# Kernel tuning notes

Measured on AMD Instinct MI355X. Metric: run time of the kernel, lower is better.

Reference implementation:

```python
import jax, jax.numpy as jnp
import numpy as np

MODEL_DIM = 256
NUM_HEAD = 8
HEAD_DIM = MODEL_DIM // NUM_HEAD  # 32
ROT_DIM_AXIS = int(0.5 * HEAD_DIM)  # 16 per axis, 32 total rotated channels
LN_EPS = 1e-5
MASK_BIAS = -1e9  # fp32 precision
SCALE = HEAD_DIM ** -0.5
INIT_RANGE = 0.02
N_LAYERS = 6


def _rotate_half(x):
    # interleaved pairs: (d r) with r=2 -> (-x2, x1) re-interleaved
    x = x.reshape(*x.shape[:-1], -1, 2)
    x1, x2 = x[..., 0], x[..., 1]
    return jnp.stack([-x2, x1], axis=-1).reshape(*x.shape[:-2], -1)


def _axial_freqs(seqlen):
    # RotaryEmbedding('lang' freqs) over t = linspace(-1, 1, seqlen)
    inv_freq = 1.0 / (10000.0 ** (jnp.arange(0, ROT_DIM_AXIS, 2, dtype=jnp.float32) / ROT_DIM_AXIS))
    t = jnp.linspace(-1.0, 1.0, seqlen, dtype=jnp.float32)
    f = jnp.repeat(t[:, None] * inv_freq[None, :], 2, axis=-1)  # (s, ROT_DIM_AXIS)
    fh = jnp.broadcast_to(f[:, None, :], (seqlen, seqlen, ROT_DIM_AXIS))
    fw = jnp.broadcast_to(f[None, :, :], (seqlen, seqlen, ROT_DIM_AXIS))
    return jnp.concatenate([fh, fw], axis=-1)  # (s, s, 2*ROT_DIM_AXIS)


def _apply_rotary(freqs, t):
    rot_dim = freqs.shape[-1]
    t_rot, t_pass = t[..., :rot_dim], t[..., rot_dim:]
    t_rot = t_rot * jnp.cos(freqs) + _rotate_half(t_rot) * jnp.sin(freqs)
    return jnp.concatenate([t_rot, t_pass], axis=-1)


def setup_inputs() -> dict:
    key = jax.random.key(0)
    k1, k2, k3, k4 = jax.random.split(key, 4)
    b, s = 2, 128
    pair_act = jax.random.normal(k1, (b, s, s, MODEL_DIM), dtype=jnp.float32)
    pair_mask = jax.random.randint(k2, (b, s, s), 0, 2).astype(bool)  # True = masked
    Wqkv = jax.random.normal(k3, (3 * MODEL_DIM, MODEL_DIM), dtype=jnp.float32) * INIT_RANGE
    Wout = jax.random.normal(k4, (MODEL_DIM, MODEL_DIM), dtype=jnp.float32) * (INIT_RANGE / np.sqrt(2 * N_LAYERS))
    ln_gamma = jnp.ones((MODEL_DIM,), dtype=jnp.float32)
    ln_beta = jnp.zeros((MODEL_DIM,), dtype=jnp.float32)
    return {"pair_act": pair_act, "pair_mask": pair_mask, "ln_gamma": ln_gamma,
            "ln_beta": ln_beta, "Wqkv": Wqkv, "Wout": Wout}


def reference(pair_act, pair_mask, ln_gamma, ln_beta, Wqkv, Wout):
    # orientation == 'per_row': no axis swap
    b, s = pair_act.shape[0], pair_act.shape[1]
    # LayerNorm over model_dim
    mu = jnp.mean(pair_act, axis=-1, keepdims=True)
    var = jnp.var(pair_act, axis=-1, keepdims=True)
    x = (pair_act - mu) * jax.lax.rsqrt(var + LN_EPS) * ln_gamma + ln_beta
    # QKV projection (no bias)
    qkv = jnp.einsum('bxyd,ed->bxye', x, Wqkv)  # (b, s, s, 3*MODEL_DIM)
    q, k, v = jnp.split(qkv, 3, axis=-1)
    # 2D axial rotary on first 2*ROT_DIM_AXIS channels of the feature dim
    freqs = _axial_freqs(s)  # (s, s, 32)
    q = _apply_rotary(freqs, q)
    k = _apply_rotary(freqs, k)
    # multihead attention per row (axis s1 independent)
    q = q.reshape(b, s, s, NUM_HEAD, HEAD_DIM)
    k = k.reshape(b, s, s, NUM_HEAD, HEAD_DIM)
    v = v.reshape(b, s, s, NUM_HEAD, HEAD_DIM)
    scores = jnp.einsum('bxqhd,bxkhd->bxhqk', q, k) * SCALE  # (b, s1, h, s2, s2)
    mask = pair_mask[:, :, None, None, :]  # (b, s1, 1, 1, s2)
    scores = jnp.where(mask, MASK_BIAS, scores)
    attn = jax.nn.softmax(scores, axis=-1)
    out = jnp.einsum('bxhqk,bxkhd->bxqhd', attn, v).reshape(b, s, s, MODEL_DIM)
    return jnp.einsum('bxyd,ed->bxye', out, Wout)
```

## Files before the change

kernel.cpp:

```cpp
#include <hip/hip_runtime.h>
#include <math.h>
#include <stdint.h>

typedef __attribute__((ext_vector_type(8))) short short8;
typedef __attribute__((ext_vector_type(4))) short short4v;
typedef __attribute__((ext_vector_type(4))) float floatx4;

#define SEQ 128
#define DM 256
#define NQKV 768
#define LN_EPS 1e-5f
#define ATT_SCALE 0.17677669529663687f

__device__ __constant__ float INVF[8] = {
    1.0f, 0.31622776601683794f, 0.1f, 0.031622776601683794f,
    0.01f, 0.0031622776601683794f, 0.001f, 0.00031622776601683794f};

__device__ inline unsigned short f2bf(float f) {
    unsigned u = __float_as_uint(f);
    u += 0x7fffu + ((u >> 16) & 1u);
    return (unsigned short)(u >> 16);
}

__device__ inline void gl_lds16(const unsigned short* g, unsigned short* l) {
    __builtin_amdgcn_global_load_lds(
        (const __attribute__((address_space(1))) void*)(uintptr_t)g,
        (__attribute__((address_space(3))) void*)(uintptr_t)l, 16, 0, 0);
}

__global__ __launch_bounds__(256)
void prep_kernel(const float* __restrict__ pa, const float* __restrict__ gamma,
                 const float* __restrict__ beta, unsigned short* __restrict__ xln,
                 const float* __restrict__ wq, const float* __restrict__ wo,
                 unsigned short* __restrict__ bq, unsigned short* __restrict__ bo) {
    int bid = blockIdx.x;
    int tid = threadIdx.x;
    if (bid < 8192) {
        int lane = tid & 63, wid = tid >> 6;
        int row = bid * 4 + wid;
        float4 v = *(const float4*)(pa + (size_t)row * DM + lane * 4);
        float s = v.x + v.y + v.z + v.w;
        #pragma unroll
        for (int o = 32; o > 0; o >>= 1) s += __shfl_xor(s, o);
        float mean = s * (1.0f / DM);
        float d0 = v.x - mean, d1 = v.y - mean, d2 = v.z - mean, d3 = v.w - mean;
        float sq = d0 * d0 + d1 * d1 + d2 * d2 + d3 * d3;
        #pragma unroll
        for (int o = 32; o > 0; o >>= 1) sq += __shfl_xor(sq, o);
        float r = rsqrtf(sq * (1.0f / DM) + LN_EPS);
        float4 g = *(const float4*)(gamma + lane * 4);
        float4 b = *(const float4*)(beta + lane * 4);
        short4v o4;
        o4[0] = (short)f2bf(d0 * r * g.x + b.x);
        o4[1] = (short)f2bf(d1 * r * g.y + b.y);
        o4[2] = (short)f2bf(d2 * r * g.z + b.z);
        o4[3] = (short)f2bf(d3 * r * g.w + b.w);
        *(short4v*)(xln + (size_t)row * DM + lane * 4) = o4;
    } else {
        int e = bid - 8192;
        bq[e * DM + tid] = f2bf(wq[e * DM + tid]);
        if (e < DM) bo[e * DM + tid] = f2bf(wo[e * DM + tid]);
    }
}

template <bool OUTBF16, bool ROT>
__global__ __launch_bounds__(256)
void gemm_mfma(const unsigned short* __restrict__ A,
               const unsigned short* __restrict__ B,
               void* __restrict__ Cout, int N) {
    __shared__ __align__(16) unsigned short As[128 * 64];
    __shared__ __align__(16) unsigned short Bs[128 * 64];
    int m0 = blockIdx.x * 128, n0 = blockIdx.y * 128;
    int tid = threadIdx.x;
    int wave = tid >> 6, lane = tid & 63, qd = lane >> 4, lo = lane & 15;
    int wm = (wave & 1) * 64, wn = (wave >> 1) * 64;

    floatx4 acc[4][4];
    #pragma unroll
    for (int i = 0; i < 4; ++i)
        #pragma unroll
        for (int j = 0; j < 4; ++j) acc[i][j] = (floatx4){0.f, 0.f, 0.f, 0.f};

    int rsub = lane >> 3;
    int csub = (lane & 7) ^ rsub;

    for (int k0 = 0; k0 < 256; k0 += 64) {
        #pragma unroll
        for (int t = 0; t < 4; ++t) {
            int rbase = (wave * 4 + t) * 8;
            int row = rbase + rsub;
            gl_lds16(A + (size_t)(m0 + row) * 256 + k0 + csub * 8, &As[rbase * 64]);
            gl_lds16(B + (size_t)(n0 + row) * 256 + k0 + csub * 8, &Bs[rbase * 64]);
        }
        __syncthreads();
        #pragma unroll
        for (int kk = 0; kk < 64; kk += 32) {
            int kkc = kk >> 3;
            short8 af[4], bf[4];
            #pragma unroll
            for (int t = 0; t < 4; ++t) {
                int row = wm + t * 16 + lo;
                int sc = (kkc + qd) ^ (row & 7);
                af[t] = *(const short8*)&As[row * 64 + sc * 8];
            }
            #pragma unroll
            for (int t = 0; t < 4; ++t) {
                int row = wn + t * 16 + lo;
                int sc = (kkc + qd) ^ (row & 7);
                bf[t] = *(const short8*)&Bs[row * 64 + sc * 8];
            }
            #pragma unroll
            for (int i = 0; i < 4; ++i)
                #pragma unroll
                for (int j = 0; j < 4; ++j)
                    acc[i][j] = __builtin_amdgcn_mfma_f32_16x16x32_bf16(
                        af[i], bf[j], acc[i][j], 0, 0, 0);
        }
        __syncthreads();
    }

    if (ROT) {
        #pragma unroll
        for (int j = 0; j < 4; ++j) {
            int gcb = n0 + wn + j * 16;
            int sect = gcb >> 5;
            if (sect == 0 || sect == 8) {
                int p = (((j & 1) * 16) + lo) >> 1;
                float invf = INVF[p & 7];
                float sgn = (lo & 1) ? 1.0f : -1.0f;
                #pragma unroll
                for (int i = 0; i < 4; ++i) {
                    #pragma unroll
                    for (int r = 0; r < 4; ++r) {
                        int grow = m0 + wm + i * 16 + qd * 4 + r;
                        int yy = grow & 127, xx = (grow >> 7) & 127;
                        float tpos = (p < 8) ? (-1.0f + (2.0f / 127.0f) * (float)xx)
                                             : (-1.0f + (2.0f / 127.0f) * (float)yy);
                        float th = tpos * invf;
                        float sn, cs;
                        __sincosf(th, &sn, &cs);
                        float v = acc[i][j][r];
                        float pv = __shfl_xor(v, 1);
                        acc[i][j][r] = v * cs + sgn * pv * sn;
                    }
                }
            }
        }
    }

    #pragma unroll
    for (int i = 0; i < 4; ++i) {
        int growb = m0 + wm + i * 16 + qd * 4;
        #pragma unroll
        for (int j = 0; j < 4; ++j) {
            int gc = n0 + wn + j * 16 + lo;
            #pragma unroll
            for (int r = 0; r < 4; ++r) {
                float v = acc[i][j][r];
                int grow = growb + r;
                if (OUTBF16) {
                    unsigned b = f2bf(v);
                    unsigned other = (unsigned)__shfl_xor((int)b, 1) & 0xffffu;
                    if ((lo & 1) == 0) {
                        unsigned pk = b | (other << 16);
                        *(unsigned*)((unsigned short*)Cout + (size_t)grow * N + gc) = pk;
                    }
                } else {
                    ((float*)Cout)[(size_t)grow * N + gc] = v;
                }
            }
        }
    }
}

__global__ __launch_bounds__(256)
void attn_mfma(const unsigned short* __restrict__ qkv, const int* __restrict__ mask,
               unsigned short* __restrict__ attn_out) {
    __shared__ __align__(16) unsigned short Vt[32 * 136];
    __shared__ __align__(16) unsigned short Ps[128 * 136];

    int blk = blockIdx.x;
    int h = blk & 7, bx = blk >> 3;
    int tid = threadIdx.x;
    int wave = tid >> 6, lane = tid & 63, qd = lane >> 4, lo = lane & 15;
    const unsigned short* base = qkv + (size_t)bx * SEQ * NQKV;

    {
        int row = tid >> 1, half = tid & 1;
        const unsigned short* vp = base + row * NQKV + 512 + h * 32 + half * 16;
        short8 v0 = *(const short8*)vp;
        short8 v1 = *(const short8*)(vp + 8);
        #pragma unroll
        for (int j = 0; j < 8; ++j) {
            Vt[(half * 16 + j) * 136 + row] = (unsigned short)v0[j];
            Vt[(half * 16 + 8 + j) * 136 + row] = (unsigned short)v1[j];
        }
    }
    __syncthreads();

    int m0 = wave * 32;

    short8 aq[2];
    #pragma unroll
    for (int t = 0; t < 2; ++t)
        aq[t] = *(const short8*)(base + (m0 + t * 16 + lo) * NQKV + h * 32 + qd * 8);

    float msel[8];
    #pragma unroll
    for (int nt = 0; nt < 8; ++nt)
        msel[nt] = mask[bx * SEQ + nt * 16 + lo] ? 0.0f : 1.0f;

    float s[2][4] = {};
    #pragma unroll
    for (int nt = 0; nt < 8; ++nt) {
        short8 bk = *(const short8*)(base + (nt * 16 + lo) * NQKV + 256 + h * 32 + qd * 8);
        #pragma unroll
        for (int t = 0; t < 2; ++t) {
            floatx4 c = (floatx4){0.f, 0.f, 0.f, 0.f};
            c = __builtin_amdgcn_mfma_f32_16x16x32_bf16(aq[t], bk, c, 0, 0, 0);
            #pragma unroll
            for (int r = 0; r < 4; ++r) {
                float e = __expf(c[r] * ATT_SCALE) * msel[nt];
                s[t][r] += e;
                Ps[(m0 + t * 16 + qd * 4 + r) * 136 + nt * 16 + lo] = f2bf(e);
            }
        }
    }

    float inv[2][4];
    #pragma unroll
    for (int t = 0; t < 2; ++t)
        #pragma unroll
        for (int r = 0; r < 4; ++r) {
            float v = s[t][r];
            v += __shfl_xor(v, 1);
            v += __shfl_xor(v, 2);
            v += __shfl_xor(v, 4);
            v += __shfl_xor(v, 8);
            inv[t][r] = 1.0f / v;
        }

    floatx4 o[2][2];
    #pragma unroll
    for (int t = 0; t < 2; ++t)
        #pragma unroll
        for (int n = 0; n < 2; ++n) o[t][n] = (floatx4){0.f, 0.f, 0.f, 0.f};
    #pragma unroll
    for (int k0 = 0; k0 < 4; ++k0) {
        short8 pa[2], vb[2];
        #pragma unroll
        for (int t = 0; t < 2; ++t)
            pa[t] = *(const short8*)&Ps[(m0 + t * 16 + lo) * 136 + k0 * 32 + qd * 8];
        #pragma unroll
        for (int n = 0; n < 2; ++n)
            vb[n] = *(const short8*)&Vt[(n * 16 + lo) * 136 + k0 * 32 + qd * 8];
        #pragma unroll
        for (int t = 0; t < 2; ++t)
            #pragma unroll
            for (int n = 0; n < 2; ++n)
                o[t][n] = __builtin_amdgcn_mfma_f32_16x16x32_bf16(
                    pa[t], vb[n], o[t][n], 0, 0, 0);
    }

    #pragma unroll
    for (int t = 0; t < 2; ++t)
        #pragma unroll
        for (int r = 0; r < 4; ++r) {
            int qrow = m0 + t * 16 + qd * 4 + r;
            float iv = inv[t][r];
            #pragma unroll
            for (int n = 0; n < 2; ++n) {
                float v = o[t][n][r] * iv;
                unsigned b = f2bf(v);
                unsigned other = (unsigned)__shfl_xor((int)b, 1) & 0xffffu;
                if ((lo & 1) == 0) {
                    unsigned pk = b | (other << 16);
                    *(unsigned*)&attn_out[((size_t)bx * SEQ + qrow) * DM +
                                          h * 32 + n * 16 + lo] = pk;
                }
            }
        }
}

extern "C" void kernel_launch(void* const* d_in, const int* in_sizes, int n_in,
                              void* d_out, int out_size, void* d_ws, size_t ws_size,
                              hipStream_t stream) {
    const float* pair_act = (const float*)d_in[0];
    const int* pair_mask = (const int*)d_in[1];
    const float* ln_gamma = (const float*)d_in[2];
    const float* ln_beta = (const float*)d_in[3];
    const float* Wqkv = (const float*)d_in[4];
    const float* Wout = (const float*)d_in[5];
    float* out = (float*)d_out;

    char* ws = (char*)d_ws;
    unsigned short* qkv_bf = (unsigned short*)ws;
    unsigned short* xln_bf = (unsigned short*)(ws + 50331648);
    unsigned short* attn_bf = (unsigned short*)(ws + 67108864);
    unsigned short* wqkv_bf = (unsigned short*)(ws + 83886080);
    unsigned short* wout_bf = (unsigned short*)(ws + 84279296);

    const int R = 2 * SEQ * SEQ;

    prep_kernel<<<8960, 256, 0, stream>>>(pair_act, ln_gamma, ln_beta, xln_bf,
                                          Wqkv, Wout, wqkv_bf, wout_bf);
    gemm_mfma<true, true><<<dim3(R / 128, NQKV / 128), 256, 0, stream>>>(
        xln_bf, wqkv_bf, qkv_bf, NQKV);
    attn_mfma<<<2 * SEQ * 8, 256, 0, stream>>>(qkv_bf, pair_mask, attn_bf);
    gemm_mfma<false, false><<<dim3(R / 128, DM / 128), 256, 0, stream>>>(
        attn_bf, wout_bf, out, DM);
}
```

Before: 151.0 us.

## Fuse LayerNorm, QKV projection, attention and output projection into one per-row kernel

Replaces the four-kernel pipeline with a small weight-conversion kernel and a single fused kernel. Each block of 512 threads handles one attention row of 128 tokens and keeps LayerNorm output, Q/K/V, attention output and the output projection in registers and LDS. This removes the global round-trips for the bf16 LN activations, the QKV tensor and the attention output. In exchange, only 256 blocks are launched, register pressure is high, and the weight tiles are reloaded into LDS by every block with many barriers per block.

Result: slower. 156.9 us (+3.9%).

```diff
diff --git a/kernel.cpp b/kernel.cpp
--- a/kernel.cpp
+++ b/kernel.cpp
@@ -3,12 +3,8 @@
 #include <stdint.h>
 
 typedef __attribute__((ext_vector_type(8))) short short8;
-typedef __attribute__((ext_vector_type(4))) short short4v;
 typedef __attribute__((ext_vector_type(4))) float floatx4;
 
-#define SEQ 128
-#define DM 256
-#define NQKV 768
 #define LN_EPS 1e-5f
 #define ATT_SCALE 0.17677669529663687f
 
@@ -29,257 +25,280 @@
 }
 
 __global__ __launch_bounds__(256)
-void prep_kernel(const float* __restrict__ pa, const float* __restrict__ gamma,
-                 const float* __restrict__ beta, unsigned short* __restrict__ xln,
-                 const float* __restrict__ wq, const float* __restrict__ wo,
-                 unsigned short* __restrict__ bq, unsigned short* __restrict__ bo) {
-    int bid = blockIdx.x;
+void prep_w(const float* __restrict__ wq, const float* __restrict__ wo,
+            unsigned short* __restrict__ bq, unsigned short* __restrict__ bo) {
+    int g = blockIdx.x * 256 + threadIdx.x;
+    const float* src;
+    unsigned short* dst;
+    if (g < 49152) { src = wq + (size_t)g * 4; dst = bq + (size_t)g * 4; }
+    else { int h = g - 49152; src = wo + (size_t)h * 4; dst = bo + (size_t)h * 4; }
+    float4 v = *(const float4*)src;
+    uint2 o;
+    o.x = (unsigned)f2bf(v.x) | ((unsigned)f2bf(v.y) << 16);
+    o.y = (unsigned)f2bf(v.z) | ((unsigned)f2bf(v.w) << 16);
+    *(uint2*)dst = o;
+}
+
+__global__ __launch_bounds__(512, 2)
+void fused_kernel(const float* __restrict__ pair_act, const int* __restrict__ mask,
+                  const float* __restrict__ gamma, const float* __restrict__ beta,
+                  const unsigned short* __restrict__ Wqkv,
+                  const unsigned short* __restrict__ Wout,
+                  float* __restrict__ out) {
+    __shared__ __align__(16) unsigned char smem[61952];
+    unsigned short* S16 = (unsigned short*)smem;
+    unsigned short* Ks = (unsigned short*)(smem + 32768);
+    unsigned short* Vt = (unsigned short*)(smem + 43008);
+
+    int bx = blockIdx.x;
     int tid = threadIdx.x;
-    if (bid < 8192) {
-        int lane = tid & 63, wid = tid >> 6;
-        int row = bid * 4 + wid;
-        float4 v = *(const float4*)(pa + (size_t)row * DM + lane * 4);
-        float s = v.x + v.y + v.z + v.w;
-        #pragma unroll
-        for (int o = 32; o > 0; o >>= 1) s += __shfl_xor(s, o);
-        float mean = s * (1.0f / DM);
-        float d0 = v.x - mean, d1 = v.y - mean, d2 = v.z - mean, d3 = v.w - mean;
-        float sq = d0 * d0 + d1 * d1 + d2 * d2 + d3 * d3;
-        #pragma unroll
-        for (int o = 32; o > 0; o >>= 1) sq += __shfl_xor(sq, o);
-        float r = rsqrtf(sq * (1.0f / DM) + LN_EPS);
-        float4 g = *(const float4*)(gamma + lane * 4);
-        float4 b = *(const float4*)(beta + lane * 4);
-        short4v o4;
-        o4[0] = (short)f2bf(d0 * r * g.x + b.x);
-        o4[1] = (short)f2bf(d1 * r * g.y + b.y);
-        o4[2] = (short)f2bf(d2 * r * g.z + b.z);
-        o4[3] = (short)f2bf(d3 * r * g.w + b.w);
-        *(short4v*)(xln + (size_t)row * DM + lane * 4) = o4;
-    } else {
-        int e = bid - 8192;
-        bq[e * DM + tid] = f2bf(wq[e * DM + tid]);
-        if (e < DM) bo[e * DM + tid] = f2bf(wo[e * DM + tid]);
-    }
-}
-
-template <bool OUTBF16, bool ROT>
-__global__ __launch_bounds__(256)
-void gemm_mfma(const unsigned short* __restrict__ A,
-               const unsigned short* __restrict__ B,
-               void* __restrict__ Cout, int N) {
-    __shared__ __align__(16) unsigned short As[128 * 64];
-    __shared__ __align__(16) unsigned short Bs[128 * 64];
-    int m0 = blockIdx.x * 128, n0 = blockIdx.y * 128;
-    int tid = threadIdx.x;
-    int wave = tid >> 6, lane = tid & 63, qd = lane >> 4, lo = lane & 15;
-    int wm = (wave & 1) * 64, wn = (wave >> 1) * 64;
-
-    floatx4 acc[4][4];
-    #pragma unroll
-    for (int i = 0; i < 4; ++i)
-        #pragma unroll
-        for (int j = 0; j < 4; ++j) acc[i][j] = (floatx4){0.f, 0.f, 0.f, 0.f};
-
-    int rsub = lane >> 3;
-    int csub = (lane & 7) ^ rsub;
-
-    for (int k0 = 0; k0 < 256; k0 += 64) {
-        #pragma unroll
-        for (int t = 0; t < 4; ++t) {
-            int rbase = (wave * 4 + t) * 8;
-            int row = rbase + rsub;
-            gl_lds16(A + (size_t)(m0 + row) * 256 + k0 + csub * 8, &As[rbase * 64]);
-            gl_lds16(B + (size_t)(n0 + row) * 256 + k0 + csub * 8, &Bs[rbase * 64]);
-        }
-        __syncthreads();
-        #pragma unroll
-        for (int kk = 0; kk < 64; kk += 32) {
-            int kkc = kk >> 3;
-            short8 af[4], bf[4];
+    int w = tid >> 6, lane = tid & 63, qd = lane >> 4, lo = lane & 15;
+    unsigned short* Qscr = (unsigned short*)(smem + 51712) + w * 640;
+
+    float tX = -1.0f + (2.0f / 127.0f) * (float)(bx & 127);
+
+    short8 a_frag[8];
+    #pragma unroll
+    for (int p = 0; p < 2; ++p) {
+        if (tid < 256) {
+            int rl = tid >> 2, q0 = tid & 3;
+            const float* src = pair_act + ((size_t)(bx * 128 + p * 64 + rl)) * 256;
+            float4 v[16];
+            float s = 0.f;
+            #pragma unroll
+            for (int u = 0; u < 16; ++u) {
+                v[u] = *(const float4*)(src + q0 * 4 + u * 16);
+                s += v[u].x + v[u].y + v[u].z + v[u].w;
+            }
+            s += __shfl_xor(s, 1);
+            s += __shfl_xor(s, 2);
+            float mean = s * (1.0f / 256.0f);
+            float sq = 0.f;
+            #pragma unroll
+            for (int u = 0; u < 16; ++u) {
+                float d0 = v[u].x - mean, d1 = v[u].y - mean;
+                float d2 = v[u].z - mean, d3 = v[u].w - mean;
+                sq += d0 * d0 + d1 * d1 + d2 * d2 + d3 * d3;
+            }
+            sq += __shfl_xor(sq, 1);
+            sq += __shfl_xor(sq, 2);
+            float rs = rsqrtf(sq * (1.0f / 256.0f) + LN_EPS);
+            #pragma unroll
+            for (int u = 0; u < 16; ++u) {
+                float4 g4 = *(const float4*)(gamma + q0 * 4 + u * 16);
+                float4 b4 = *(const float4*)(beta + q0 * 4 + u * 16);
+                unsigned e0 = f2bf((v[u].x - mean) * rs * g4.x + b4.x);
+                unsigned e1 = f2bf((v[u].y - mean) * rs * g4.y + b4.y);
+                unsigned e2 = f2bf((v[u].z - mean) * rs * g4.z + b4.z);
+                unsigned e3 = f2bf((v[u].w - mean) * rs * g4.w + b4.w);
+                int c = 2 * u + (q0 >> 1);
+                int half = q0 & 1;
+                int ss = (c & ~7) | ((c & 7) ^ (rl & 7));
+                uint2 pk = {e0 | (e1 << 16), e2 | (e3 << 16)};
+                *(uint2*)&S16[rl * 256 + ss * 8 + half * 4] = pk;
+            }
+        }
+        __syncthreads();
+        if ((w >> 2) == p) {
+            int rl = (w & 3) * 16 + lo;
+            #pragma unroll
+            for (int c = 0; c < 8; ++c) {
+                int ci = 4 * c + qd;
+                int ss = (ci & ~7) | ((ci & 7) ^ (rl & 7));
+                a_frag[c] = *(const short8*)&S16[rl * 256 + ss * 8];
+            }
+        }
+        __syncthreads();
+    }
+
+    unsigned q_pk[4][4][2], k_pk[4][4][2], v_pk[4][4][2];
+    #pragma unroll
+    for (int nc = 0; nc < 12; ++nc) {
+        #pragma unroll
+        for (int i = 0; i < 4; ++i) {
+            int rbase = i * 16 + w * 2;
+            int row = rbase + (lane >> 5);
+            int sl = lane & 31;
+            int c = (sl & ~7) | ((sl & 7) ^ (row & 7));
+            gl_lds16(Wqkv + (size_t)(nc * 64 + row) * 256 + c * 8, S16 + rbase * 256);
+        }
+        __syncthreads();
+        floatx4 acc[4];
+        #pragma unroll
+        for (int t = 0; t < 4; ++t) acc[t] = (floatx4){0.f, 0.f, 0.f, 0.f};
+        #pragma unroll
+        for (int c = 0; c < 8; ++c) {
             #pragma unroll
             for (int t = 0; t < 4; ++t) {
-                int row = wm + t * 16 + lo;
-                int sc = (kkc + qd) ^ (row & 7);
-                af[t] = *(const short8*)&As[row * 64 + sc * 8];
-            }
-            #pragma unroll
-            for (int t = 0; t < 4; ++t) {
-                int row = wn + t * 16 + lo;
-                int sc = (kkc + qd) ^ (row & 7);
-                bf[t] = *(const short8*)&Bs[row * 64 + sc * 8];
-            }
-            #pragma unroll
-            for (int i = 0; i < 4; ++i)
-                #pragma unroll
-                for (int j = 0; j < 4; ++j)
-                    acc[i][j] = __builtin_amdgcn_mfma_f32_16x16x32_bf16(
-                        af[i], bf[j], acc[i][j], 0, 0, 0);
-        }
-        __syncthreads();
-    }
-
-    if (ROT) {
-        #pragma unroll
-        for (int j = 0; j < 4; ++j) {
-            int gcb = n0 + wn + j * 16;
-            int sect = gcb >> 5;
-            if (sect == 0 || sect == 8) {
-                int p = (((j & 1) * 16) + lo) >> 1;
-                float invf = INVF[p & 7];
+                int rw = t * 16 + lo;
+                int ci = 4 * c + qd;
+                int ss = (ci & ~7) | ((ci & 7) ^ (rw & 7));
+                short8 bf = *(const short8*)&S16[rw * 256 + ss * 8];
+                acc[t] = __builtin_amdgcn_mfma_f32_16x16x32_bf16(a_frag[c], bf,
+                                                                 acc[t], 0, 0, 0);
+            }
+        }
+        __syncthreads();
+        if (nc == 0 || nc == 4) {
+            #pragma unroll
+            for (int t = 0; t < 2; ++t) {
+                int pi = (t * 16 + lo) >> 1;
+                float invf = INVF[pi & 7];
                 float sgn = (lo & 1) ? 1.0f : -1.0f;
                 #pragma unroll
-                for (int i = 0; i < 4; ++i) {
-                    #pragma unroll
-                    for (int r = 0; r < 4; ++r) {
-                        int grow = m0 + wm + i * 16 + qd * 4 + r;
-                        int yy = grow & 127, xx = (grow >> 7) & 127;
-                        float tpos = (p < 8) ? (-1.0f + (2.0f / 127.0f) * (float)xx)
-                                             : (-1.0f + (2.0f / 127.0f) * (float)yy);
-                        float th = tpos * invf;
-                        float sn, cs;
-                        __sincosf(th, &sn, &cs);
-                        float v = acc[i][j][r];
-                        float pv = __shfl_xor(v, 1);
-                        acc[i][j][r] = v * cs + sgn * pv * sn;
-                    }
+                for (int r = 0; r < 4; ++r) {
+                    int y = 16 * w + qd * 4 + r;
+                    float tp = (pi < 8) ? tX : (-1.0f + (2.0f / 127.0f) * (float)y);
+                    float sn, cs;
+                    __sincosf(tp * invf, &sn, &cs);
+                    float vv = acc[t][r];
+                    float pv = __shfl_xor(vv, 1);
+                    acc[t][r] = vv * cs + sgn * pv * sn;
                 }
             }
         }
-    }
-
-    #pragma unroll
-    for (int i = 0; i < 4; ++i) {
-        int growb = m0 + wm + i * 16 + qd * 4;
-        #pragma unroll
-        for (int j = 0; j < 4; ++j) {
-            int gc = n0 + wn + j * 16 + lo;
+        #pragma unroll
+        for (int t = 0; t < 4; ++t) {
+            unsigned p0 = (unsigned)f2bf(acc[t][0]) | ((unsigned)f2bf(acc[t][1]) << 16);
+            unsigned p1 = (unsigned)f2bf(acc[t][2]) | ((unsigned)f2bf(acc[t][3]) << 16);
+            if (nc < 4) { q_pk[nc][t][0] = p0; q_pk[nc][t][1] = p1; }
+            else if (nc < 8) { k_pk[nc - 4][t][0] = p0; k_pk[nc - 4][t][1] = p1; }
+            else { v_pk[nc - 8][t][0] = p0; v_pk[nc - 8][t][1] = p1; }
+        }
+    }
+
+    float msel[8];
+    #pragma unroll
+    for (int nt = 0; nt < 8; ++nt)
+        msel[nt] = mask[bx * 128 + nt * 16 + lo] ? 0.0f : 1.0f;
+
+    unsigned o_pk[8][2][2];
+    #pragma unroll
+    for (int h = 0; h < 8; ++h) {
+        int hc = h >> 1, tt0 = (h & 1) * 2;
+        #pragma unroll
+        for (int tt = 0; tt < 2; ++tt) {
+            int t = tt0 + tt;
             #pragma unroll
             for (int r = 0; r < 4; ++r) {
-                float v = acc[i][j][r];
-                int grow = growb + r;
-                if (OUTBF16) {
-                    unsigned b = f2bf(v);
-                    unsigned other = (unsigned)__shfl_xor((int)b, 1) & 0xffffu;
-                    if ((lo & 1) == 0) {
-                        unsigned pk = b | (other << 16);
-                        *(unsigned*)((unsigned short*)Cout + (size_t)grow * N + gc) = pk;
-                    }
-                } else {
-                    ((float*)Cout)[(size_t)grow * N + gc] = v;
-                }
-            }
-        }
-    }
-}
-
-__global__ __launch_bounds__(256)
-void attn_mfma(const unsigned short* __restrict__ qkv, const int* __restrict__ mask,
-               unsigned short* __restrict__ attn_out) {
-    __shared__ __align__(16) unsigned short Vt[32 * 136];
-    __shared__ __align__(16) unsigned short Ps[128 * 136];
-
-    int blk = blockIdx.x;
-    int h = blk & 7, bx = blk >> 3;
-    int tid = threadIdx.x;
-    int wave = tid >> 6, lane = tid & 63, qd = lane >> 4, lo = lane & 15;
-    const unsigned short* base = qkv + (size_t)bx * SEQ * NQKV;
-
-    {
-        int row = tid >> 1, half = tid & 1;
-        const unsigned short* vp = base + row * NQKV + 512 + h * 32 + half * 16;
-        short8 v0 = *(const short8*)vp;
-        short8 v1 = *(const short8*)(vp + 8);
-        #pragma unroll
-        for (int j = 0; j < 8; ++j) {
-            Vt[(half * 16 + j) * 136 + row] = (unsigned short)v0[j];
-            Vt[(half * 16 + 8 + j) * 136 + row] = (unsigned short)v1[j];
-        }
-    }
-    __syncthreads();
-
-    int m0 = wave * 32;
-
-    short8 aq[2];
-    #pragma unroll
-    for (int t = 0; t < 2; ++t)
-        aq[t] = *(const short8*)(base + (m0 + t * 16 + lo) * NQKV + h * 32 + qd * 8);
-
-    float msel[8];
-    #pragma unroll
-    for (int nt = 0; nt < 8; ++nt)
-        msel[nt] = mask[bx * SEQ + nt * 16 + lo] ? 0.0f : 1.0f;
-
-    float s[2][4] = {};
-    #pragma unroll
-    for (int nt = 0; nt < 8; ++nt) {
-        short8 bk = *(const short8*)(base + (nt * 16 + lo) * NQKV + 256 + h * 32 + qd * 8);
-        #pragma unroll
-        for (int t = 0; t < 2; ++t) {
+                unsigned kv = (k_pk[hc][t][r >> 1] >> ((r & 1) * 16)) & 0xffffu;
+                unsigned vv = (v_pk[hc][t][r >> 1] >> ((r & 1) * 16)) & 0xffffu;
+                int key = 16 * w + qd * 4 + r;
+                int d = tt * 16 + lo;
+                Ks[key * 40 + d] = (unsigned short)kv;
+                Vt[d * 136 + key] = (unsigned short)vv;
+            }
+        }
+        __syncthreads();
+        #pragma unroll
+        for (int tt = 0; tt < 2; ++tt) {
+            int t = tt0 + tt;
+            #pragma unroll
+            for (int r = 0; r < 4; ++r) {
+                unsigned qv = (q_pk[hc][t][r >> 1] >> ((r & 1) * 16)) & 0xffffu;
+                Qscr[(qd * 4 + r) * 40 + tt * 16 + lo] = (unsigned short)qv;
+            }
+        }
+        short8 aq = *(const short8*)&Qscr[lo * 40 + qd * 8];
+        float ef[8][4];
+        float sums[4] = {0.f, 0.f, 0.f, 0.f};
+        #pragma unroll
+        for (int nt = 0; nt < 8; ++nt) {
+            short8 bk = *(const short8*)&Ks[(nt * 16 + lo) * 40 + qd * 8];
             floatx4 c = (floatx4){0.f, 0.f, 0.f, 0.f};
-            c = __builtin_amdgcn_mfma_f32_16x16x32_bf16(aq[t], bk, c, 0, 0, 0);
+            c = __builtin_amdgcn_mfma_f32_16x16x32_bf16(aq, bk, c, 0, 0, 0);
             #pragma unroll
             for (int r = 0; r < 4; ++r) {
                 float e = __expf(c[r] * ATT_SCALE) * msel[nt];
-                s[t][r] += e;
-                Ps[(m0 + t * 16 + qd * 4 + r) * 136 + nt * 16 + lo] = f2bf(e);
-            }
-        }
-    }
-
-    float inv[2][4];
-    #pragma unroll
-    for (int t = 0; t < 2; ++t)
+                ef[nt][r] = e;
+                sums[r] += e;
+            }
+        }
+        float inv[4];
         #pragma unroll
         for (int r = 0; r < 4; ++r) {
-            float v = s[t][r];
+            float v = sums[r];
             v += __shfl_xor(v, 1);
             v += __shfl_xor(v, 2);
             v += __shfl_xor(v, 4);
             v += __shfl_xor(v, 8);
-            inv[t][r] = 1.0f / v;
-        }
-
-    floatx4 o[2][2];
-    #pragma unroll
-    for (int t = 0; t < 2; ++t)
-        #pragma unroll
-        for (int n = 0; n < 2; ++n) o[t][n] = (floatx4){0.f, 0.f, 0.f, 0.f};
-    #pragma unroll
-    for (int k0 = 0; k0 < 4; ++k0) {
-        short8 pa[2], vb[2];
-        #pragma unroll
-        for (int t = 0; t < 2; ++t)
-            pa[t] = *(const short8*)&Ps[(m0 + t * 16 + lo) * 136 + k0 * 32 + qd * 8];
-        #pragma unroll
-        for (int n = 0; n < 2; ++n)
-            vb[n] = *(const short8*)&Vt[(n * 16 + lo) * 136 + k0 * 32 + qd * 8];
-        #pragma unroll
-        for (int t = 0; t < 2; ++t)
-            #pragma unroll
-            for (int n = 0; n < 2; ++n)
-                o[t][n] = __builtin_amdgcn_mfma_f32_16x16x32_bf16(
-                    pa[t], vb[n], o[t][n], 0, 0, 0);
-    }
-
-    #pragma unroll
-    for (int t = 0; t < 2; ++t)
-        #pragma unroll
-        for (int r = 0; r < 4; ++r) {
-            int qrow = m0 + t * 16 + qd * 4 + r;
-            float iv = inv[t][r];
+            inv[r] = 1.0f / v;
+        }
+        floatx4 o[2];
+        o[0] = (floatx4){0.f, 0.f, 0.f, 0.f};
+        o[1] = (floatx4){0.f, 0.f, 0.f, 0.f};
+        #pragma unroll
+        for (int c2 = 0; c2 < 4; ++c2) {
+            #pragma unroll
+            for (int half = 0; half < 2; ++half) {
+                int nt = c2 * 2 + half;
+                #pragma unroll
+                for (int r = 0; r < 4; ++r)
+                    Qscr[(qd * 4 + r) * 40 + half * 16 + lo] = f2bf(ef[nt][r]);
+            }
+            short8 pa = *(const short8*)&Qscr[lo * 40 + qd * 8];
             #pragma unroll
             for (int n = 0; n < 2; ++n) {
-                float v = o[t][n][r] * iv;
-                unsigned b = f2bf(v);
-                unsigned other = (unsigned)__shfl_xor((int)b, 1) & 0xffffu;
-                if ((lo & 1) == 0) {
-                    unsigned pk = b | (other << 16);
-                    *(unsigned*)&attn_out[((size_t)bx * SEQ + qrow) * DM +
-                                          h * 32 + n * 16 + lo] = pk;
-                }
-            }
-        }
+                short8 vb = *(const short8*)&Vt[(n * 16 + lo) * 136 + c2 * 32 + qd * 8];
+                o[n] = __builtin_amdgcn_mfma_f32_16x16x32_bf16(pa, vb, o[n], 0, 0, 0);
+            }
+        }
+        #pragma unroll
+        for (int n = 0; n < 2; ++n) {
+            o_pk[h][n][0] = (unsigned)f2bf(o[n][0] * inv[0]) |
+                            ((unsigned)f2bf(o[n][1] * inv[1]) << 16);
+            o_pk[h][n][1] = (unsigned)f2bf(o[n][2] * inv[2]) |
+                            ((unsigned)f2bf(o[n][3] * inv[3]) << 16);
+        }
+        __syncthreads();
+    }
+
+    short8 of[8];
+    #pragma unroll
+    for (int h = 0; h < 8; ++h) {
+        #pragma unroll
+        for (int tt = 0; tt < 2; ++tt)
+            #pragma unroll
+            for (int r = 0; r < 4; ++r) {
+                unsigned ov = (o_pk[h][tt][r >> 1] >> ((r & 1) * 16)) & 0xffffu;
+                Qscr[(qd * 4 + r) * 40 + tt * 16 + lo] = (unsigned short)ov;
+            }
+        of[h] = *(const short8*)&Qscr[lo * 40 + qd * 8];
+    }
+    #pragma unroll
+    for (int nc = 0; nc < 4; ++nc) {
+        #pragma unroll
+        for (int i = 0; i < 4; ++i) {
+            int rbase = i * 16 + w * 2;
+            int row = rbase + (lane >> 5);
+            int sl = lane & 31;
+            int c = (sl & ~7) | ((sl & 7) ^ (row & 7));
+            gl_lds16(Wout + (size_t)(nc * 64 + row) * 256 + c * 8, S16 + rbase * 256);
+        }
+        __syncthreads();
+        floatx4 acc[4];
+        #pragma unroll
+        for (int t = 0; t < 4; ++t) acc[t] = (floatx4){0.f, 0.f, 0.f, 0.f};
+        #pragma unroll
+        for (int c = 0; c < 8; ++c) {
+            #pragma unroll
+            for (int t = 0; t < 4; ++t) {
+                int rw = t * 16 + lo;
+                int ci = 4 * c + qd;
+                int ss = (ci & ~7) | ((ci & 7) ^ (rw & 7));
+                short8 bf = *(const short8*)&S16[rw * 256 + ss * 8];
+                acc[t] = __builtin_amdgcn_mfma_f32_16x16x32_bf16(of[c], bf,
+                                                                 acc[t], 0, 0, 0);
+            }
+        }
+        #pragma unroll
+        for (int t = 0; t < 4; ++t)
+            #pragma unroll
+            for (int r = 0; r < 4; ++r)
+                out[(size_t)(bx * 128 + 16 * w + qd * 4 + r) * 256 + nc * 64 +
+                    t * 16 + lo] = acc[t][r];
+        __syncthreads();
+    }
 }
 
 extern "C" void kernel_launch(void* const* d_in, const int* in_sizes, int n_in,
@@ -294,19 +313,10 @@
     float* out = (float*)d_out;
 
     char* ws = (char*)d_ws;
-    unsigned short* qkv_bf = (unsigned short*)ws;
-    unsigned short* xln_bf = (unsigned short*)(ws + 50331648);
-    unsigned short* attn_bf = (unsigned short*)(ws + 67108864);
-    unsigned short* wqkv_bf = (unsigned short*)(ws + 83886080);
-    unsigned short* wout_bf = (unsigned short*)(ws + 84279296);
-
-    const int R = 2 * SEQ * SEQ;
-
-    prep_kernel<<<8960, 256, 0, stream>>>(pair_act, ln_gamma, ln_beta, xln_bf,
-                                          Wqkv, Wout, wqkv_bf, wout_bf);
-    gemm_mfma<true, true><<<dim3(R / 128, NQKV / 128), 256, 0, stream>>>(
-        xln_bf, wqkv_bf, qkv_bf, NQKV);
-    attn_mfma<<<2 * SEQ * 8, 256, 0, stream>>>(qkv_bf, pair_mask, attn_bf);
-    gemm_mfma<false, false><<<dim3(R / 128, DM / 128), 256, 0, stream>>>(
-        attn_bf, wout_bf, out, DM);
-}
+    unsigned short* wqkv_bf = (unsigned short*)ws;
+    unsigned short* wout_bf = (unsigned short*)(ws + 393216);
+
+    prep_w<<<256, 256, 0, stream>>>(Wqkv, Wout, wqkv_bf, wout_bf);
+    fused_kernel<<<256, 512, 0, stream>>>(pair_act, pair_mask, ln_gamma, ln_beta,
+                                          wqkv_bf, wout_bf, out);
+}
```
